# Performance work log

Hardware: AMD Instinct MI355X
Metric: run time of the kernel (lower is better)

## Reference

```python
import jax, jax.numpy as jnp
import numpy as np

B, C, H, W = 4, 128, 64, 64
CI = C // 2  # inter_channels
BN_EPS = 1e-5


def _conv1x1(x, w, b):
    # x: [B,C,H,W], w: [O,C], b: [O] -> [B,O,H,W]
    return jnp.einsum('bchw,oc->bohw', x, w) + b[None, :, None, None]


def setup_inputs() -> dict:
    key = jax.random.key(0)
    ks = jax.random.split(key, 11)
    s_in = 1.0 / np.sqrt(C)
    s_mid = 1.0 / np.sqrt(CI)
    return {
        'x': jax.random.normal(ks[0], (B, C, H, W), dtype=jnp.float32),
        'g_w': jax.random.normal(ks[1], (CI, C), dtype=jnp.float32) * s_in,
        'g_b': jax.random.normal(ks[2], (CI,), dtype=jnp.float32) * 0.01,
        'theta_w': jax.random.normal(ks[3], (CI, C), dtype=jnp.float32) * s_in,
        'theta_b': jax.random.normal(ks[4], (CI,), dtype=jnp.float32) * 0.01,
        'phi_w': jax.random.normal(ks[5], (CI, C), dtype=jnp.float32) * s_in,
        'phi_b': jax.random.normal(ks[6], (CI,), dtype=jnp.float32) * 0.01,
        'w_w': jax.random.normal(ks[7], (C, CI), dtype=jnp.float32) * s_mid,
        'w_b': jax.random.normal(ks[8], (C,), dtype=jnp.float32) * 0.01,
        'bn_gamma': jnp.ones((C,), dtype=jnp.float32),
        'bn_beta': jnp.zeros((C,), dtype=jnp.float32),
    }


def reference(x, g_w, g_b, theta_w, theta_b, phi_w, phi_b, w_w, w_b, bn_gamma, bn_beta):
    b, c, h, w = x.shape
    n = h * w
    # 1x1 conv projections, flattened over spatial positions -> [B,N,CI]
    g_x = _conv1x1(x, g_w, g_b).reshape(b, CI, n).transpose(0, 2, 1)
    theta_x = _conv1x1(x, theta_w, theta_b).reshape(b, CI, n).transpose(0, 2, 1)
    phi_x = _conv1x1(x, phi_w, phi_b).reshape(b, CI, n)  # [B,CI,N]
    # full attention over spatial tokens: [B,N,N]
    f = jnp.einsum('bnc,bcm->bnm', theta_x, phi_x)
    f_div_c = jax.nn.softmax(f, axis=-1)
    y = jnp.einsum('bnm,bmc->bnc', f_div_c, g_x)  # [B,N,CI]
    y = y.transpose(0, 2, 1).reshape(b, CI, h, w)
    w_y = _conv1x1(y, w_w, w_b)  # [B,C,H,W]
    # BatchNorm2d (training-mode batch statistics over B,H,W)
    mean = jnp.mean(w_y, axis=(0, 2, 3))
    var = jnp.var(w_y, axis=(0, 2, 3))
    bn = bn_gamma[None, :, None, None] * (w_y - mean[None, :, None, None]) \
         * jax.lax.rsqrt(var + BN_EPS)[None, :, None, None] + bn_beta[None, :, None, None]
    return bn + x
```

## Files before the change

kernel.cpp:

```cpp
#include <hip/hip_runtime.h>
#include <hip/hip_bf16.h>
#include <math.h>

#define NSP 4096
#define CC  128
#define CIC 64
#define NB  4
#define LOG2E 1.4426950408889634f

typedef unsigned short u16;
typedef unsigned int u32;
typedef short s8bf __attribute__((ext_vector_type(8)));
typedef float f32x4 __attribute__((ext_vector_type(4)));
typedef float f32x2 __attribute__((ext_vector_type(2)));
typedef float f32x16 __attribute__((ext_vector_type(16)));

#define MFMA32(a, b, c) __builtin_amdgcn_mfma_f32_32x32x16_bf16(a, b, c, 0, 0, 0)

#define WSB_PB    0
#define WSB_TH    (NB * CIC * NSP * 2)
#define WSB_PH    (WSB_TH + NB * NSP * CIC * 2)
#define WSB_OP    (WSB_PH + NB * NSP * CIC * 2)
#define WSB_LP    (WSB_OP + (size_t)NB * 2 * NSP * CIC * 4)
#define WSB_WT4   (WSB_LP + NB * 2 * NSP * 4)
#define WSB_WT2P  (WSB_WT4 + CC * 256 * 4)
#define WSB_PARTS (WSB_WT2P + CIC * CC * 4)

__device__ __forceinline__ u16 f2bf(float f) {
    union { float f; unsigned u; } v; v.f = f;
    unsigned r = v.u + 0x7fffu + ((v.u >> 16) & 1u);
    return (u16)(r >> 16);
}

__global__ __launch_bounds__(256) void prep_kernel(
    const float* __restrict__ g_w, const float* __restrict__ t_w,
    const float* __restrict__ p_w, const float* __restrict__ w_w,
    float* __restrict__ wT4, float* __restrict__ wT2p)
{
    const int c = blockIdx.x;
    const int o = threadIdx.x;
    if (o < 192) {
        float v;
        if (o < 64)       v = g_w[o * CC + c];
        else if (o < 128) v = t_w[(o - 64) * CC + c] * LOG2E;
        else              v = p_w[(o - 128) * CC + c];
        wT4[(c << 8) + ((o & 63) << 2) + (o >> 6)] = v;
    } else {
        wT4[(c << 8) + ((o - 192) << 2) + 3] = 0.f;
    }
    if (o < CIC)
        wT2p[(o << 7) + ((c & 63) << 1) + (c >> 6)] = w_w[c * CIC + o];
}

__global__ __launch_bounds__(512) void proj_kernel(
    const float* __restrict__ x, const float* __restrict__ wT4,
    const float* __restrict__ g_b, const float* __restrict__ t_b,
    const float* __restrict__ p_b,
    u16* __restrict__ PB, u16* __restrict__ th_tm, u16* __restrict__ ph_tm)
{
    __shared__ float Xs[CC][36];
    __shared__ u16 Ot[192][40];

    const int b    = blockIdx.y;
    const int n0   = blockIdx.x * 32;
    const int tid  = threadIdx.x;
    const int lane = tid & 63;
    const int wv   = tid >> 6;
    const int t0   = wv * 4;

    const float* xb = x + (size_t)b * CC * NSP + n0;
    #pragma unroll
    for (int k = 0; k < 2; ++k) {
        int idx = tid + (k << 9);
        int c = idx >> 3, t4 = (idx & 7) << 2;
        *(f32x4*)&Xs[c][t4] = *(const f32x4*)(xb + (size_t)c * NSP + t4);
    }
    __syncthreads();

    float acc[3][4];
    {
        float b0 = g_b[lane], b1 = t_b[lane] * LOG2E, b2 = p_b[lane];
        #pragma unroll
        for (int t = 0; t < 4; ++t) { acc[0][t] = b0; acc[1][t] = b1; acc[2][t] = b2; }
    }

    const float* wp = wT4 + (lane << 2);
    #pragma unroll 8
    for (int c = 0; c < CC; ++c) {
        f32x4 wv4 = *(const f32x4*)(wp + (c << 8));
        f32x4 xv  = *(const f32x4*)&Xs[c][t0];
        #pragma unroll
        for (int t = 0; t < 4; ++t) {
            acc[0][t] += wv4[0] * xv[t];
            acc[1][t] += wv4[1] * xv[t];
            acc[2][t] += wv4[2] * xv[t];
        }
    }

    #pragma unroll
    for (int p = 0; p < 3; ++p) {
        #pragma unroll
        for (int i = 0; i < 2; ++i) {
            unsigned pk = (unsigned)f2bf(acc[p][2 * i]) | ((unsigned)f2bf(acc[p][2 * i + 1]) << 16);
            *(unsigned*)&Ot[lane + 64 * p][t0 + 2 * i] = pk;
        }
    }
    __syncthreads();

    if (tid < 256) {
        int row = tid >> 2, ch = tid & 3;
        uint4 v = *(const uint4*)&Ot[row][ch * 8];
        *(uint4*)(PB + (size_t)b * CIC * NSP + (size_t)row * NSP + n0 + ch * 8) = v;
    }
    {
        int tok = tid >> 4, sel = (tid >> 3) & 1, c8 = (tid & 7) * 8;
        u16* dst = (sel ? ph_tm : th_tm) + ((size_t)b * NSP + n0 + tok) * 64 + c8;
        union { u16 t[8]; uint4 v4; } u;
        #pragma unroll
        for (int j = 0; j < 8; ++j) u.t[j] = Ot[64 + sel * 64 + c8 + j][tok];
        *(uint4*)dst = u.v4;
    }
}

__global__ __launch_bounds__(512, 2) void attn_kernel(
    const u16* __restrict__ PB, const u16* __restrict__ th_tm,
    const u16* __restrict__ ph_tm,
    float* __restrict__ O_part, float* __restrict__ l_part)
{
    const int b    = blockIdx.z;
    const int kvs  = blockIdx.y;
    const int q0   = blockIdx.x << 7;
    const int tid  = threadIdx.x;
    const int lane = tid & 63;
    const int w    = tid >> 6;
    const int s    = w & 3;
    const int h    = w >> 2;
    const int l31  = lane & 31;
    const int l5   = lane >> 5;

    __shared__ __align__(16) char KV[2][2][2][8192];

    const u16* gp = PB + (size_t)b * CIC * NSP;
    const u16* th = th_tm + (size_t)b * NSP * 64;
    const u16* ph = ph_tm + (size_t)b * NSP * 64;

    const int kb0 = kvs << 11;

    const int srow = tid >> 3;
    const int scol = tid & 7;
    const int ldst = srow * 128 + (((scol ^ (srow & 7)) & 7) << 4);

    float4 rK0, rK1, rV0, rV1;
    auto load_t = [&](int t) {
        const int m0 = kb0 + (t << 6);
        rK0 = *(const float4*)(ph + ((size_t)(m0 + srow) << 6) + (scol << 3));
        rK1 = *(const float4*)(ph + ((size_t)(m0 + 1024 + srow) << 6) + (scol << 3));
        rV0 = *(const float4*)(gp + (size_t)srow * NSP + m0 + (scol << 3));
        rV1 = *(const float4*)(gp + (size_t)srow * NSP + m0 + 1024 + (scol << 3));
    };
    auto write_t = [&](int buf) {
        *(float4*)(&KV[buf][0][0][0] + ldst) = rK0;
        *(float4*)(&KV[buf][0][1][0] + ldst) = rK1;
        *(float4*)(&KV[buf][1][0][0] + ldst) = rV0;
        *(float4*)(&KV[buf][1][1][0] + ldst) = rV1;
    };

    s8bf qb[4];
    const int qtok = q0 + (s << 5) + l31;
    #pragma unroll
    for (int fc = 0; fc < 4; ++fc)
        qb[fc] = *(const s8bf*)(th + ((size_t)qtok << 6) + fc * 16 + l5 * 8);

    f32x16 Ov0, Ov1, cinit;
    #pragma unroll
    for (int i = 0; i < 16; ++i) { Ov0[i] = 0.f; Ov1[i] = 0.f; cinit[i] = -32.f; }
    float lr = 0.f;

    load_t(0); write_t(0); load_t(1);
    __syncthreads();

    u32 pk[2][4][2];

    for (int t = 0; t < 16; ++t) {
        const int buf = t & 1;

        if (t < 15) write_t(buf ^ 1);
        if (t < 14) load_t(t + 2);

        const char* Kb = &KV[buf][0][h][0];
        const char* Vb = &KV[buf][1][h][0];

        #pragma unroll
        for (int kt = 0; kt < 2; ++kt) {
            const int trow = l31 + (kt << 5);
            const int rswz = trow & 7;
            f32x16 sv = cinit;
            __builtin_amdgcn_s_setprio(1);
            #pragma unroll
            for (int fc = 0; fc < 4; ++fc) {
                s8bf ka = *(const s8bf*)(Kb + trow * 128 + (((2 * fc + l5) ^ rswz) << 4));
                sv = MFMA32(ka, qb[fc], sv);
            }
            __builtin_amdgcn_s_setprio(0);
            float e[16];
            #pragma unroll
            for (int i = 0; i < 16; ++i) e[i] = __builtin_amdgcn_exp2f(sv[i]);
            #pragma unroll
            for (int i = 0; i < 16; ++i) lr += e[i];
            #pragma unroll
            for (int m = 0; m < 4; ++m) {
                #pragma unroll
                for (int i = 0; i < 2; ++i) {
                    __hip_bfloat162 hh = __float22bfloat162_rn(
                        make_float2(e[4 * m + 2 * i], e[4 * m + 2 * i + 1]));
                    union { __hip_bfloat162 h2; u32 u; } cv; cv.h2 = hh;
                    pk[kt][m][i] = cv.u;
                }
            }
        }

        __builtin_amdgcn_s_setprio(1);
        #pragma unroll
        for (int f = 0; f < 4; ++f) {
            const int tt = f >> 1;
            const int m0c = 2 * (f & 1);
            u32 sA0 = pk[tt][m0c][0],     sA1 = pk[tt][m0c][1];
            u32 sB0 = pk[tt][m0c + 1][0], sB1 = pk[tt][m0c + 1][1];
            u32 self0 = l5 ? sB0 : sA0, self1 = l5 ? sB1 : sA1;
            u32 send0 = l5 ? sA0 : sB0, send1 = l5 ? sA1 : sB1;
            u32 x0 = (u32)__shfl_xor((int)send0, 32);
            u32 x1 = (u32)__shfl_xor((int)send1, 32);
            union { u32 u[4]; s8bf v; } pa;
            pa.u[0] = l5 ? x0 : self0;
            pa.u[1] = l5 ? x1 : self1;
            pa.u[2] = l5 ? self0 : x0;
            pa.u[3] = l5 ? self1 : x1;
            const int c1 = l31 + 32;
            s8bf v0 = *(const s8bf*)(Vb + l31 * 128 + (((2 * f + l5) ^ (l31 & 7)) << 4));
            s8bf v1 = *(const s8bf*)(Vb + c1 * 128 + (((2 * f + l5) ^ (c1 & 7)) << 4));
            Ov0 = MFMA32(pa.v, v0, Ov0);
            Ov1 = MFMA32(pa.v, v1, Ov1);
        }
        __builtin_amdgcn_s_setprio(0);

        __syncthreads();
    }

    float lrh = lr + __shfl_xor(lr, 32);
    float* Olds = (float*)&KV[0][0][0][0];
    float* Llds = (float*)&KV[1][0][0][0];

    if (h == 1) {
        #pragma unroll
        for (int reg = 0; reg < 16; ++reg) {
            int q = (reg & 3) + 8 * (reg >> 2) + 4 * l5;
            Olds[((s << 5) + q) * 64 + l31]      = Ov0[reg];
            Olds[((s << 5) + q) * 64 + 32 + l31] = Ov1[reg];
        }
        if (l5 == 0) Llds[(s << 5) + l31] = lrh;
    }
    __syncthreads();
    if (h == 0) {
        float ltot = lrh + Llds[(s << 5) + l31];
        float* Ob = O_part + ((size_t)b * 2 + kvs) * NSP * 64;
        #pragma unroll
        for (int reg = 0; reg < 16; ++reg) {
            int q = (reg & 3) + 8 * (reg >> 2) + 4 * l5;
            int qg = q0 + (s << 5) + q;
            Ob[(size_t)qg * 64 + l31]      = Ov0[reg] + Olds[((s << 5) + q) * 64 + l31];
            Ob[(size_t)qg * 64 + 32 + l31] = Ov1[reg] + Olds[((s << 5) + q) * 64 + 32 + l31];
        }
        if (l5 == 0)
            l_part[((size_t)b * 2 + kvs) * NSP + q0 + (s << 5) + l31] = ltot;
    }
}

__global__ __launch_bounds__(256) void wconv_kernel(
    const float* __restrict__ O_part, const float* __restrict__ l_part,
    const float* __restrict__ wT2p, const float* __restrict__ w_b,
    float* __restrict__ out)
{
    __shared__ float Ys[CIC][36];
    __shared__ float Of[CC][36];

    const int b    = blockIdx.y;
    const int n0   = blockIdx.x * 32;
    const int tid  = threadIdx.x;
    const int lane = tid & 63;
    const int wv   = tid >> 6;
    const int t0   = wv * 8;

    #pragma unroll
    for (int rnd = 0; rnd < 2; ++rnd) {
        int tok = (tid >> 4) + (rnd << 4);
        int ci4 = tid & 15;
        int qg  = n0 + tok;
        f32x4 a = {0.f, 0.f, 0.f, 0.f};
        float ls = 0.f;
        #pragma unroll
        for (int kvs = 0; kvs < 2; ++kvs) {
            a += *(const f32x4*)(O_part + (((size_t)b * 2 + kvs) * NSP + qg) * 64 + (ci4 << 2));
            ls += l_part[((size_t)b * 2 + kvs) * NSP + qg];
        }
        float inv = 1.0f / ls;
        #pragma unroll
        for (int j = 0; j < 4; ++j) Ys[(ci4 << 2) + j][tok] = a[j] * inv;
    }
    __syncthreads();

    float acc[2][8];
    #pragma unroll
    for (int t = 0; t < 8; ++t) { acc[0][t] = 0.f; acc[1][t] = 0.f; }

    const float* wp = wT2p + (lane << 1);
    #pragma unroll 8
    for (int ci = 0; ci < CIC; ++ci) {
        f32x2 wv2 = *(const f32x2*)(wp + (ci << 7));
        f32x4 y0 = *(const f32x4*)&Ys[ci][t0];
        f32x4 y1 = *(const f32x4*)&Ys[ci][t0 + 4];
        #pragma unroll
        for (int t = 0; t < 4; ++t) {
            acc[0][t]     += wv2[0] * y0[t];
            acc[0][4 + t] += wv2[0] * y1[t];
            acc[1][t]     += wv2[1] * y0[t];
            acc[1][4 + t] += wv2[1] * y1[t];
        }
    }

    float b0 = w_b[lane], b1 = w_b[64 + lane];
    #pragma unroll
    for (int t = 0; t < 4; ++t) {
        Of[lane][t0 + t]          = acc[0][t] + b0;
        Of[lane][t0 + 4 + t]      = acc[0][4 + t] + b0;
        Of[64 + lane][t0 + t]     = acc[1][t] + b1;
        Of[64 + lane][t0 + 4 + t] = acc[1][4 + t] + b1;
    }
    __syncthreads();

    float* ob = out + (size_t)b * CC * NSP + n0;
    #pragma unroll
    for (int k = 0; k < 4; ++k) {
        int idx = tid + (k << 8);
        int row = idx >> 3, ch = idx & 7;
        *(float4*)(ob + (size_t)row * NSP + ch * 4) = *(const float4*)&Of[row][ch * 4];
    }
}

__global__ __launch_bounds__(256) void stats_kernel(
    const float* __restrict__ wy, float* __restrict__ parts)
{
    const int c   = blockIdx.x >> 2;
    const int qd  = blockIdx.x & 3;
    const int tid = threadIdx.x;
    float s = 0.f, ss = 0.f;
    #pragma unroll 4
    for (int k = 0; k < 16; ++k) {
        int i = qd * 4096 + k * 256 + tid;
        int b = i >> 12, n = i & (NSP - 1);
        float v = wy[((size_t)b * CC + c) * NSP + n];
        s += v; ss += v * v;
    }
    #pragma unroll
    for (int off = 32; off > 0; off >>= 1) {
        s  += __shfl_down(s, off, 64);
        ss += __shfl_down(ss, off, 64);
    }
    __shared__ float sred[4], ssred[4];
    const int wid = tid >> 6, lane = tid & 63;
    if (lane == 0) { sred[wid] = s; ssred[wid] = ss; }
    __syncthreads();
    if (tid == 0) {
        parts[(c * 4 + qd) * 2]     = sred[0] + sred[1] + sred[2] + sred[3];
        parts[(c * 4 + qd) * 2 + 1] = ssred[0] + ssred[1] + ssred[2] + ssred[3];
    }
}

__global__ __launch_bounds__(256) void bn_kernel(
    const float* __restrict__ x, const float* __restrict__ parts,
    const float* __restrict__ gamma, const float* __restrict__ beta,
    float* __restrict__ out)
{
    const int i = blockIdx.x * 256 + threadIdx.x;
    const int c = (i >> 10) & (CC - 1);
    float s  = parts[c * 8]     + parts[c * 8 + 2] + parts[c * 8 + 4] + parts[c * 8 + 6];
    float ss = parts[c * 8 + 1] + parts[c * 8 + 3] + parts[c * 8 + 5] + parts[c * 8 + 7];
    float mean = s * (1.0f / 16384.0f);
    float var  = ss * (1.0f / 16384.0f) - mean * mean;
    float istd = rsqrtf(var + 1e-5f);
    float ga = gamma[c] * istd;
    float be = beta[c] - mean * ga;
    float4 wy = ((const float4*)out)[i];
    float4 xv = ((const float4*)x)[i];
    float4 o;
    o.x = wy.x * ga + be + xv.x;
    o.y = wy.y * ga + be + xv.y;
    o.z = wy.z * ga + be + xv.z;
    o.w = wy.w * ga + be + xv.w;
    ((float4*)out)[i] = o;
}

extern "C" void kernel_launch(void* const* d_in, const int* in_sizes, int n_in,
                              void* d_out, int out_size, void* d_ws, size_t ws_size,
                              hipStream_t stream)
{
    const float* x    = (const float*)d_in[0];
    const float* g_w  = (const float*)d_in[1];
    const float* g_b  = (const float*)d_in[2];
    const float* t_w  = (const float*)d_in[3];
    const float* t_b  = (const float*)d_in[4];
    const float* p_w  = (const float*)d_in[5];
    const float* p_b  = (const float*)d_in[6];
    const float* w_w  = (const float*)d_in[7];
    const float* w_b  = (const float*)d_in[8];
    const float* bn_g = (const float*)d_in[9];
    const float* bn_b = (const float*)d_in[10];
    float* out = (float*)d_out;
    char* ws8  = (char*)d_ws;

    u16*   PB    = (u16*)(ws8 + WSB_PB);
    u16*   TH    = (u16*)(ws8 + WSB_TH);
    u16*   PH    = (u16*)(ws8 + WSB_PH);
    float* OP    = (float*)(ws8 + WSB_OP);
    float* LP    = (float*)(ws8 + WSB_LP);
    float* wT4   = (float*)(ws8 + WSB_WT4);
    float* wT2p  = (float*)(ws8 + WSB_WT2P);
    float* parts = (float*)(ws8 + WSB_PARTS);

    prep_kernel <<<dim3(CC), 256, 0, stream>>>(g_w, t_w, p_w, w_w, wT4, wT2p);
    proj_kernel <<<dim3(NSP / 32, NB), 512, 0, stream>>>(x, wT4, g_b, t_b, p_b, PB, TH, PH);
    attn_kernel <<<dim3(NSP / 128, 2, NB), 512, 0, stream>>>(PB, TH, PH, OP, LP);
    wconv_kernel<<<dim3(NSP / 32, NB), 256, 0, stream>>>(OP, LP, wT2p, w_b, out);
    stats_kernel<<<dim3(CC * 4), 256, 0, stream>>>(out, parts);
    bn_kernel   <<<dim3(2048), 256, 0, stream>>>(x, parts, bn_g, bn_b, out);
}
```

Before: 76.30 us.

## Give each attention wave two query tiles and halve the block size

The attention kernel now runs 256 threads (4 waves) per block instead of 512. Each wave handles two 32-token query tiles that share every K and V fragment read from LDS, and the KV tile per iteration shrinks to 32 keys over 32 iterations with a new V swizzle. The aim is to halve LDS traffic per MFMA through register-level reuse of K/V. In exchange it doubles the accumulator registers per wave, leaves fewer waves to hide latency, and adds more sync iterations.

```diff
diff --git a/kernel.cpp b/kernel.cpp
--- a/kernel.cpp
+++ b/kernel.cpp
@@ -122,7 +122,7 @@
     }
 }
 
-__global__ __launch_bounds__(512, 2) void attn_kernel(
+__global__ __launch_bounds__(256, 2) void attn_kernel(
     const u16* __restrict__ PB, const u16* __restrict__ th_tm,
     const u16* __restrict__ ph_tm,
     float* __restrict__ O_part, float* __restrict__ l_part)
@@ -133,12 +133,13 @@
     const int tid  = threadIdx.x;
     const int lane = tid & 63;
     const int w    = tid >> 6;
-    const int s    = w & 3;
-    const int h    = w >> 2;
+    const int s    = w & 1;
+    const int h    = w >> 1;
     const int l31  = lane & 31;
     const int l5   = lane >> 5;
 
-    __shared__ __align__(16) char KV[2][2][2][8192];
+    __shared__ __align__(16) char KVb[2][2][2][4096];
+    __shared__ float Lm[128];
 
     const u16* gp = PB + (size_t)b * CIC * NSP;
     const u16* th = th_tm + (size_t)b * NSP * 64;
@@ -146,132 +147,189 @@
 
     const int kb0 = kvs << 11;
 
-    const int srow = tid >> 3;
-    const int scol = tid & 7;
-    const int ldst = srow * 128 + (((scol ^ (srow & 7)) & 7) << 4);
+    const int krow = tid >> 3;
+    const int kch  = tid & 7;
+    const int vrow = tid >> 2;
+    const int vch  = tid & 3;
+    const int kdst = krow * 128 + (((kch ^ (krow & 7)) & 7) << 4);
+    const int vdst = vrow * 64  + ((vch ^ (vrow & 3)) << 4);
 
     float4 rK0, rK1, rV0, rV1;
     auto load_t = [&](int t) {
-        const int m0 = kb0 + (t << 6);
-        rK0 = *(const float4*)(ph + ((size_t)(m0 + srow) << 6) + (scol << 3));
-        rK1 = *(const float4*)(ph + ((size_t)(m0 + 1024 + srow) << 6) + (scol << 3));
-        rV0 = *(const float4*)(gp + (size_t)srow * NSP + m0 + (scol << 3));
-        rV1 = *(const float4*)(gp + (size_t)srow * NSP + m0 + 1024 + (scol << 3));
+        const int m0 = kb0 + (t << 5);
+        rK0 = *(const float4*)(ph + ((size_t)(m0 + krow) << 6) + (kch << 3));
+        rK1 = *(const float4*)(ph + ((size_t)(m0 + 1024 + krow) << 6) + (kch << 3));
+        rV0 = *(const float4*)(gp + (size_t)vrow * NSP + m0 + (vch << 3));
+        rV1 = *(const float4*)(gp + (size_t)vrow * NSP + m0 + 1024 + (vch << 3));
     };
     auto write_t = [&](int buf) {
-        *(float4*)(&KV[buf][0][0][0] + ldst) = rK0;
-        *(float4*)(&KV[buf][0][1][0] + ldst) = rK1;
-        *(float4*)(&KV[buf][1][0][0] + ldst) = rV0;
-        *(float4*)(&KV[buf][1][1][0] + ldst) = rV1;
+        *(float4*)(&KVb[buf][0][0][0] + kdst) = rK0;
+        *(float4*)(&KVb[buf][0][1][0] + kdst) = rK1;
+        *(float4*)(&KVb[buf][1][0][0] + vdst) = rV0;
+        *(float4*)(&KVb[buf][1][1][0] + vdst) = rV1;
     };
 
-    s8bf qb[4];
-    const int qtok = q0 + (s << 5) + l31;
-    #pragma unroll
-    for (int fc = 0; fc < 4; ++fc)
-        qb[fc] = *(const s8bf*)(th + ((size_t)qtok << 6) + fc * 16 + l5 * 8);
-
-    f32x16 Ov0, Ov1, cinit;
-    #pragma unroll
-    for (int i = 0; i < 16; ++i) { Ov0[i] = 0.f; Ov1[i] = 0.f; cinit[i] = -32.f; }
-    float lr = 0.f;
+    s8bf qb0[4], qb1[4];
+    {
+        const int qt0 = q0 + (s << 6) + l31;
+        const int qt1 = qt0 + 32;
+        #pragma unroll
+        for (int fc = 0; fc < 4; ++fc) {
+            qb0[fc] = *(const s8bf*)(th + ((size_t)qt0 << 6) + fc * 16 + l5 * 8);
+            qb1[fc] = *(const s8bf*)(th + ((size_t)qt1 << 6) + fc * 16 + l5 * 8);
+        }
+    }
+
+    f32x16 Ov00, Ov01, Ov10, Ov11, cinit;
+    #pragma unroll
+    for (int i = 0; i < 16; ++i) {
+        Ov00[i] = 0.f; Ov01[i] = 0.f; Ov10[i] = 0.f; Ov11[i] = 0.f;
+        cinit[i] = -32.f;
+    }
+    float lr0 = 0.f, lr1 = 0.f;
 
     load_t(0); write_t(0); load_t(1);
     __syncthreads();
 
-    u32 pk[2][4][2];
-
-    for (int t = 0; t < 16; ++t) {
+    u32 pk0[4][2], pk1[4][2];
+    const int krd = l31 * 128;
+    const int ksw = l31 & 7;
+    const int vrd0 = l31 * 64;
+    const int vrd1 = (l31 + 32) * 64;
+    const int vsw = l31 & 3;
+
+    for (int t = 0; t < 32; ++t) {
         const int buf = t & 1;
 
-        if (t < 15) write_t(buf ^ 1);
-        if (t < 14) load_t(t + 2);
-
-        const char* Kb = &KV[buf][0][h][0];
-        const char* Vb = &KV[buf][1][h][0];
-
-        #pragma unroll
-        for (int kt = 0; kt < 2; ++kt) {
-            const int trow = l31 + (kt << 5);
-            const int rswz = trow & 7;
-            f32x16 sv = cinit;
-            __builtin_amdgcn_s_setprio(1);
-            #pragma unroll
-            for (int fc = 0; fc < 4; ++fc) {
-                s8bf ka = *(const s8bf*)(Kb + trow * 128 + (((2 * fc + l5) ^ rswz) << 4));
-                sv = MFMA32(ka, qb[fc], sv);
-            }
-            __builtin_amdgcn_s_setprio(0);
+        if (t < 31) write_t(buf ^ 1);
+        if (t < 30) load_t(t + 2);
+
+        const char* Kb = &KVb[buf][0][h][0];
+        const char* Vb = &KVb[buf][1][h][0];
+
+        f32x16 sv0 = cinit, sv1 = cinit;
+        __builtin_amdgcn_s_setprio(1);
+        #pragma unroll
+        for (int fc = 0; fc < 4; ++fc) {
+            s8bf ka = *(const s8bf*)(Kb + krd + (((2 * fc + l5) ^ ksw) << 4));
+            sv0 = MFMA32(ka, qb0[fc], sv0);
+            sv1 = MFMA32(ka, qb1[fc], sv1);
+        }
+        __builtin_amdgcn_s_setprio(0);
+
+        {
             float e[16];
             #pragma unroll
-            for (int i = 0; i < 16; ++i) e[i] = __builtin_amdgcn_exp2f(sv[i]);
-            #pragma unroll
-            for (int i = 0; i < 16; ++i) lr += e[i];
-            #pragma unroll
-            for (int m = 0; m < 4; ++m) {
+            for (int i = 0; i < 16; ++i) e[i] = __builtin_amdgcn_exp2f(sv0[i]);
+            #pragma unroll
+            for (int i = 0; i < 16; ++i) lr0 += e[i];
+            #pragma unroll
+            for (int m = 0; m < 4; ++m)
                 #pragma unroll
                 for (int i = 0; i < 2; ++i) {
                     __hip_bfloat162 hh = __float22bfloat162_rn(
                         make_float2(e[4 * m + 2 * i], e[4 * m + 2 * i + 1]));
                     union { __hip_bfloat162 h2; u32 u; } cv; cv.h2 = hh;
-                    pk[kt][m][i] = cv.u;
+                    pk0[m][i] = cv.u;
                 }
+        }
+        {
+            float e[16];
+            #pragma unroll
+            for (int i = 0; i < 16; ++i) e[i] = __builtin_amdgcn_exp2f(sv1[i]);
+            #pragma unroll
+            for (int i = 0; i < 16; ++i) lr1 += e[i];
+            #pragma unroll
+            for (int m = 0; m < 4; ++m)
+                #pragma unroll
+                for (int i = 0; i < 2; ++i) {
+                    __hip_bfloat162 hh = __float22bfloat162_rn(
+                        make_float2(e[4 * m + 2 * i], e[4 * m + 2 * i + 1]));
+                    union { __hip_bfloat162 h2; u32 u; } cv; cv.h2 = hh;
+                    pk1[m][i] = cv.u;
+                }
+        }
+
+        __builtin_amdgcn_s_setprio(1);
+        #pragma unroll
+        for (int f = 0; f < 2; ++f) {
+            s8bf v0 = *(const s8bf*)(Vb + vrd0 + (((2 * f + l5) ^ vsw) << 4));
+            s8bf v1 = *(const s8bf*)(Vb + vrd1 + (((2 * f + l5) ^ vsw) << 4));
+            {
+                u32 sA0 = pk0[2 * f][0],     sA1 = pk0[2 * f][1];
+                u32 sB0 = pk0[2 * f + 1][0], sB1 = pk0[2 * f + 1][1];
+                u32 self0 = l5 ? sB0 : sA0, self1 = l5 ? sB1 : sA1;
+                u32 send0 = l5 ? sA0 : sB0, send1 = l5 ? sA1 : sB1;
+                u32 x0 = (u32)__shfl_xor((int)send0, 32);
+                u32 x1 = (u32)__shfl_xor((int)send1, 32);
+                union { u32 u[4]; s8bf v; } pa;
+                pa.u[0] = l5 ? x0 : self0;
+                pa.u[1] = l5 ? x1 : self1;
+                pa.u[2] = l5 ? self0 : x0;
+                pa.u[3] = l5 ? self1 : x1;
+                Ov00 = MFMA32(pa.v, v0, Ov00);
+                Ov01 = MFMA32(pa.v, v1, Ov01);
             }
-        }
-
-        __builtin_amdgcn_s_setprio(1);
-        #pragma unroll
-        for (int f = 0; f < 4; ++f) {
-            const int tt = f >> 1;
-            const int m0c = 2 * (f & 1);
-            u32 sA0 = pk[tt][m0c][0],     sA1 = pk[tt][m0c][1];
-            u32 sB0 = pk[tt][m0c + 1][0], sB1 = pk[tt][m0c + 1][1];
-            u32 self0 = l5 ? sB0 : sA0, self1 = l5 ? sB1 : sA1;
-            u32 send0 = l5 ? sA0 : sB0, send1 = l5 ? sA1 : sB1;
-            u32 x0 = (u32)__shfl_xor((int)send0, 32);
-            u32 x1 = (u32)__shfl_xor((int)send1, 32);
-            union { u32 u[4]; s8bf v; } pa;
-            pa.u[0] = l5 ? x0 : self0;
-            pa.u[1] = l5 ? x1 : self1;
-            pa.u[2] = l5 ? self0 : x0;
-            pa.u[3] = l5 ? self1 : x1;
-            const int c1 = l31 + 32;
-            s8bf v0 = *(const s8bf*)(Vb + l31 * 128 + (((2 * f + l5) ^ (l31 & 7)) << 4));
-            s8bf v1 = *(const s8bf*)(Vb + c1 * 128 + (((2 * f + l5) ^ (c1 & 7)) << 4));
-            Ov0 = MFMA32(pa.v, v0, Ov0);
-            Ov1 = MFMA32(pa.v, v1, Ov1);
+            {
+                u32 sA0 = pk1[2 * f][0],     sA1 = pk1[2 * f][1];
+                u32 sB0 = pk1[2 * f + 1][0], sB1 = pk1[2 * f + 1][1];
+                u32 self0 = l5 ? sB0 : sA0, self1 = l5 ? sB1 : sA1;
+                u32 send0 = l5 ? sA0 : sB0, send1 = l5 ? sA1 : sB1;
+                u32 x0 = (u32)__shfl_xor((int)send0, 32);
+                u32 x1 = (u32)__shfl_xor((int)send1, 32);
+                union { u32 u[4]; s8bf v; } pa;
+                pa.u[0] = l5 ? x0 : self0;
+                pa.u[1] = l5 ? x1 : self1;
+                pa.u[2] = l5 ? self0 : x0;
+                pa.u[3] = l5 ? self1 : x1;
+                Ov10 = MFMA32(pa.v, v0, Ov10);
+                Ov11 = MFMA32(pa.v, v1, Ov11);
+            }
         }
         __builtin_amdgcn_s_setprio(0);
 
         __syncthreads();
     }
 
-    float lrh = lr + __shfl_xor(lr, 32);
-    float* Olds = (float*)&KV[0][0][0][0];
-    float* Llds = (float*)&KV[1][0][0][0];
+    float lrh0 = lr0 + __shfl_xor(lr0, 32);
+    float lrh1 = lr1 + __shfl_xor(lr1, 32);
+    float* Olds = (float*)&KVb[0][0][0][0];
 
     if (h == 1) {
         #pragma unroll
         for (int reg = 0; reg < 16; ++reg) {
             int q = (reg & 3) + 8 * (reg >> 2) + 4 * l5;
-            Olds[((s << 5) + q) * 64 + l31]      = Ov0[reg];
-            Olds[((s << 5) + q) * 64 + 32 + l31] = Ov1[reg];
-        }
-        if (l5 == 0) Llds[(s << 5) + l31] = lrh;
+            int r0 = (s << 6) + q;
+            Olds[(r0)*64 + l31]           = Ov00[reg];
+            Olds[(r0)*64 + 32 + l31]      = Ov01[reg];
+            Olds[(r0 + 32) * 64 + l31]      = Ov10[reg];
+            Olds[(r0 + 32) * 64 + 32 + l31] = Ov11[reg];
+        }
+        if (l5 == 0) {
+            Lm[(s << 6) + l31]      = lrh0;
+            Lm[(s << 6) + 32 + l31] = lrh1;
+        }
     }
     __syncthreads();
     if (h == 0) {
-        float ltot = lrh + Llds[(s << 5) + l31];
+        float lt0 = lrh0 + Lm[(s << 6) + l31];
+        float lt1 = lrh1 + Lm[(s << 6) + 32 + l31];
         float* Ob = O_part + ((size_t)b * 2 + kvs) * NSP * 64;
         #pragma unroll
         for (int reg = 0; reg < 16; ++reg) {
             int q = (reg & 3) + 8 * (reg >> 2) + 4 * l5;
-            int qg = q0 + (s << 5) + q;
-            Ob[(size_t)qg * 64 + l31]      = Ov0[reg] + Olds[((s << 5) + q) * 64 + l31];
-            Ob[(size_t)qg * 64 + 32 + l31] = Ov1[reg] + Olds[((s << 5) + q) * 64 + 32 + l31];
-        }
-        if (l5 == 0)
-            l_part[((size_t)b * 2 + kvs) * NSP + q0 + (s << 5) + l31] = ltot;
+            int r0 = (s << 6) + q;
+            int qg0 = q0 + r0, qg1 = q0 + r0 + 32;
+            Ob[(size_t)qg0 * 64 + l31]      = Ov00[reg] + Olds[(r0)*64 + l31];
+            Ob[(size_t)qg0 * 64 + 32 + l31] = Ov01[reg] + Olds[(r0)*64 + 32 + l31];
+            Ob[(size_t)qg1 * 64 + l31]      = Ov10[reg] + Olds[(r0 + 32) * 64 + l31];
+            Ob[(size_t)qg1 * 64 + 32 + l31] = Ov11[reg] + Olds[(r0 + 32) * 64 + 32 + l31];
+        }
+        if (l5 == 0) {
+            float* Lb = l_part + ((size_t)b * 2 + kvs) * NSP + q0;
+            Lb[(s << 6) + l31]      = lt0;
+            Lb[(s << 6) + 32 + l31] = lt1;
+        }
     }
 }
 
@@ -428,7 +486,7 @@
 
     prep_kernel <<<dim3(CC), 256, 0, stream>>>(g_w, t_w, p_w, w_w, wT4, wT2p);
     proj_kernel <<<dim3(NSP / 32, NB), 512, 0, stream>>>(x, wT4, g_b, t_b, p_b, PB, TH, PH);
-    attn_kernel <<<dim3(NSP / 128, 2, NB), 512, 0, stream>>>(PB, TH, PH, OP, LP);
+    attn_kernel <<<dim3(NSP / 128, 2, NB), 256, 0, stream>>>(PB, TH, PH, OP, LP);
     wconv_kernel<<<dim3(NSP / 32, NB), 256, 0, stream>>>(OP, LP, wT2p, w_b, out);
     stats_kernel<<<dim3(CC * 4), 256, 0, stream>>>(out, parts);
     bn_kernel   <<<dim3(2048), 256, 0, stream>>>(x, parts, bn_g, bn_b, out);
```

Result: slower. 81.53 us (+6.8%).
